# Optimization experiments

Hardware: AMD Instinct MI355X
Metric: run time of the kernel (lower is better)

Reference implementation:

```python
import jax, jax.numpy as jnp
import numpy as np

BOUND = 1.0
N_RAYS = 2048
TOT = 128        # num_steps (samples per pixel)
IND_S = 16       # indicator_steps
MAX_DEPTHS = 2
HID = 64
EPS = 1e-8


def setup_inputs() -> dict:
    key = jax.random.key(0)
    ks = jax.random.split(key, 13)
    M = N_RAYS * TOT
    rays_o = 0.3 * jax.random.normal(ks[0], (N_RAYS, 3), jnp.float32)
    rd = jax.random.normal(ks[1], (N_RAYS, 3), jnp.float32)
    rays_d = rd / (jnp.linalg.norm(rd, axis=-1, keepdims=True) + EPS)
    env_map = 0.1 * jax.random.normal(ks[2], (3, 128, 256), jnp.float32)
    Wd1 = jax.random.normal(ks[3], (3, HID), jnp.float32) / np.sqrt(3.0)
    Wd2 = jax.random.normal(ks[4], (HID, 3), jnp.float32) / np.sqrt(HID)
    Wf1 = jax.random.normal(ks[5], (6, HID), jnp.float32) / np.sqrt(6.0)
    Ws = jax.random.normal(ks[6], (HID, 3), jnp.float32) / np.sqrt(HID)
    Wdir = jax.random.normal(ks[7], (HID, 3), jnp.float32) / np.sqrt(HID)
    Wrho = jax.random.normal(ks[8], (HID, 3), jnp.float32) / np.sqrt(HID)
    jitter = jax.random.uniform(ks[9], (MAX_DEPTHS, M, IND_S), jnp.float32)
    u_t = jax.random.uniform(ks[10], (MAX_DEPTHS, M), jnp.float32)
    u_scatter = jax.random.uniform(ks[11], (MAX_DEPTHS, M), jnp.float32)
    channel = jax.random.randint(ks[12], (MAX_DEPTHS, M), 0, 3)
    return dict(rays_o=rays_o, rays_d=rays_d, env_map=env_map, Wd1=Wd1, Wd2=Wd2,
                Wf1=Wf1, Ws=Ws, Wdir=Wdir, Wrho=Wrho,
                jitter=jitter, u_t=u_t, u_scatter=u_scatter, channel=channel)


def _density(pts, Wd1, Wd2):
    # stand-in NeRF density field: 3 spectral channels, positive
    return jax.nn.softplus(jnp.sin(pts @ Wd1) @ Wd2)


def _material(o, d, Wf1, Ws, Wdir, Wrho):
    f = jnp.tanh(jnp.concatenate([o, d], axis=-1) @ Wf1)
    sigma_t = jax.nn.softplus(f @ Ws)                     # [M,3]
    dn = f @ Wdir
    d_out = dn / (jnp.linalg.norm(dn, axis=-1, keepdims=True) + EPS)
    fused_rho = jax.nn.sigmoid(f @ Wrho)                  # [M,3]
    return sigma_t, d_out, fused_rho


def _sample_env(env_map, p):
    # equirectangular lookup == torch grid_sample(bilinear, align_corners=False, zero pad)
    x, y, z = p[:, 0], p[:, 1], p[:, 2]
    theta = jnp.nan_to_num(jnp.arctan2(x, -z)) / jnp.pi            # grid x in [-1,1]
    phi = 2.0 / jnp.pi * jnp.nan_to_num(jnp.arccos(y)) - 1.0       # grid y in [-1,1]
    C, H, W = env_map.shape
    ix = ((theta + 1.0) * W - 1.0) * 0.5
    iy = ((phi + 1.0) * H - 1.0) * 0.5
    x0 = jnp.floor(ix); y0 = jnp.floor(iy)
    wx = ix - x0; wy = iy - y0

    def tap(xc, yc, w):
        inb = (xc >= 0) & (xc < W) & (yc >= 0) & (yc < H)
        xi = jnp.clip(xc, 0, W - 1).astype(jnp.int32)
        yi = jnp.clip(yc, 0, H - 1).astype(jnp.int32)
        return (w * inb)[:, None] * env_map[:, yi, xi].T   # [M,3]

    v = (tap(x0, y0, (1 - wx) * (1 - wy)) + tap(x0 + 1, y0, wx * (1 - wy)) +
         tap(x0, y0 + 1, (1 - wx) * wy) + tap(x0 + 1, y0 + 1, wx * wy))
    return jnp.exp(v)


def _render(rays_o, rays_d, env_map, Wd1, Wd2, Wf1, Ws, Wdir, Wrho,
            jitter, u_t, u_scatter, channel):
    M = N_RAYS * TOT
    o = jnp.repeat(rays_o, TOT, axis=0)   # [M,3]
    d = jnp.repeat(rays_d, TOT, axis=0)
    alive = jnp.ones((M,), bool)          # masked version of boolean compaction
    thr = jnp.ones((M, 3), jnp.float32)
    rgbs = jnp.zeros((M, 3), jnp.float32)
    lin = jnp.linspace(0.0, 1.0, IND_S)

    for dep in range(MAX_DEPTHS):
        # ray-sphere intersection (radius=bound)
        a = jnp.sum(d * d, -1)
        b = 2.0 * jnp.sum(d * o, -1)
        c = jnp.sum(o * o, -1) - BOUND ** 2
        delta = b * b - 4.0 * a * c
        alive = alive & (delta > 0.0)
        sq = jnp.sqrt(jnp.maximum(delta, 0.0))
        nears = jnp.maximum((-b - sq) / (2.0 * a), 0.001)
        fars = jnp.maximum((-b + sq) / (2.0 * a), 0.001)
        span = fars - nears

        # stratified indicator samples -> per-channel majorant
        z = nears[:, None] + span[:, None] * lin[None, :]
        z = z + (jitter[dep] - 0.5) * (span[:, None] / IND_S)
        pts = o[:, None, :] + d[:, None, :] * z[:, :, None]          # [M,S,3]
        sigma = _density(pts.reshape(-1, 3), Wd1, Wd2).reshape(M, IND_S, 3)
        ch = channel[dep]
        maj_multi = jnp.maximum(sigma.max(axis=1), 0.001)            # [M,3]
        sig_ch = jnp.take_along_axis(sigma, ch[:, None, None], axis=2)[..., 0]
        maj = jnp.maximum(sig_ch.max(axis=1), 0.001)                 # [M]

        # free-flight sampling (last depth forces hit at far boundary)
        if dep < MAX_DEPTHS - 1:
            t = -jnp.log1p(-u_t[dep]) / maj + nears
        else:
            t = fars
        hit = alive & (t >= fars)

        # environment hit contribution
        denom = jnp.exp(-maj_multi * span[:, None]) / (maj_multi.max(-1, keepdims=True) + EPS) + EPS
        Le = _sample_env(env_map, o + d * fars[:, None])
        contrib = thr * (denom / jax.lax.stop_gradient(denom.mean(-1, keepdims=True))) * Le
        rgbs = rgbs + jnp.where(hit[:, None], contrib, 0.0)
        alive = alive & ~hit
        if dep == MAX_DEPTHS - 1:
            break

        # throughput update + null/real scattering (delta tracking)
        trans = jnp.exp(-maj_multi * (t - nears)[:, None]) / maj_multi.max(-1, keepdims=True)
        den2 = jax.lax.stop_gradient((maj_multi * trans).mean(-1, keepdims=True))
        thr = jnp.where(alive[:, None], thr * trans / den2, thr)
        o = jnp.where(alive[:, None], jax.lax.stop_gradient(o + d * t[:, None]), o)
        sigma_t, d_out, fused_rho = _material(o, d, Wf1, Ws, Wdir, Wrho)
        sp = jnp.minimum(jnp.take_along_axis(sigma_t, ch[:, None], axis=1)[:, 0] / maj, 1.0)
        sm = alive & (u_scatter[dep] < sp)
        d = jnp.where(sm[:, None], d_out, d)
        thr = jnp.where(sm[:, None], thr / (sp[:, None] + EPS) * fused_rho,
              jnp.where(alive[:, None], thr / (1.0 - sp[:, None] + EPS), thr))

    return rgbs.reshape(N_RAYS, TOT, 3).mean(axis=1)   # [N,3]


def reference(rays_o, rays_d, env_map, Wd1, Wd2, Wf1, Ws, Wdir, Wrho,
              jitter, u_t, u_scatter, channel):
    return _render(rays_o, rays_d, env_map, Wd1, Wd2, Wf1, Ws, Wdir, Wrho,
                   jitter, u_t, u_scatter, channel)
```

## Files before the change

### kernel.cpp

```cpp
#include <hip/hip_runtime.h>
#include <math.h>

#define NRAYS 2048
#define TOT   128
#define INDS  16
#define HID   64
#define EPSF  1e-8f
#define MTOT  (NRAYS*TOT)
#define NTAB  128

typedef float f32x2 __attribute__((ext_vector_type(2)));
typedef float f32x4 __attribute__((ext_vector_type(4)));

__device__ __forceinline__ float softplus_f(float x) {
    return fmaxf(x, 0.0f) + __logf(1.0f + __expf(-fabsf(x)));
}
__device__ __forceinline__ float sigmoid_f(float x) {
    return 1.0f / (1.0f + __expf(-x));
}
__device__ __forceinline__ float tanh_fast(float x) {
    float e2 = __expf(2.0f * x);
    return 1.0f - 2.0f / (e2 + 1.0f);
}
__device__ __forceinline__ f32x2 pkmax(f32x2 a, f32x2 b) {
    f32x2 r; r.x = fmaxf(a.x, b.x); r.y = fmaxf(a.y, b.y); return r;
}
__device__ __forceinline__ f32x2 pkfma(f32x2 a, f32x2 b, f32x2 c) {
    return __builtin_elementwise_fma(a, b, c);
}

#define CK(i) ((float)(i)*(1.0f/15.0f) - 0.03125f)

#define MAKE_Z(jA, jB, kbase, nears, span)                                    \
    float s16 = (span) * (1.0f/16.0f);                                        \
    f32x2 z01, z23, z45, z67;                                                 \
    z01.x = fmaf((jA).x, s16, fmaf(span, CK((kbase)+0), nears));              \
    z01.y = fmaf((jA).y, s16, fmaf(span, CK((kbase)+1), nears));              \
    z23.x = fmaf((jA).z, s16, fmaf(span, CK((kbase)+2), nears));              \
    z23.y = fmaf((jA).w, s16, fmaf(span, CK((kbase)+3), nears));              \
    z45.x = fmaf((jB).x, s16, fmaf(span, CK((kbase)+4), nears));              \
    z45.y = fmaf((jB).y, s16, fmaf(span, CK((kbase)+5), nears));              \
    z67.x = fmaf((jB).z, s16, fmaf(span, CK((kbase)+6), nears));              \
    z67.y = fmaf((jB).w, s16, fmaf(span, CK((kbase)+7), nears));

#define TAB_EVAL(zz, mx0, mx1, mx2)                                           \
    {                                                                         \
        float x = ((zz) - ztab0) * invh;                                      \
        x = fminf(fmaxf(x, 0.0f), (float)(NTAB-1) - 1e-3f);                   \
        int i = (int)x; float w = x - (float)i;                               \
        float ta0 = sT0[i], tb0 = sT0[i+1];                                   \
        float ta1 = sT1[i], tb1 = sT1[i+1];                                   \
        float ta2 = sT2[i], tb2 = sT2[i+1];                                   \
        mx0 = fmaxf(mx0, fmaf(w, tb0 - ta0, ta0));                            \
        mx1 = fmaxf(mx1, fmaf(w, tb1 - ta1, ta1));                            \
        mx2 = fmaxf(mx2, fmaf(w, tb2 - ta2, ta2));                            \
    }

__device__ __forceinline__ void env_logv(
    const float* __restrict__ env_map,
    float px, float py, float pz,
    float& v0, float& v1, float& v2)
{
    float theta = atan2f(px, -pz) * (1.0f/3.14159265358979323846f);
    float acv = (fabsf(py) <= 1.0f) ? acosf(py) : 0.0f;
    float phi = 0.63661977236758134308f * acv - 1.0f;
    float ixf = ((theta + 1.0f)*256.0f - 1.0f)*0.5f;
    float iyf = ((phi   + 1.0f)*128.0f - 1.0f)*0.5f;
    float x0f = floorf(ixf), y0f = floorf(iyf);
    float wx = ixf - x0f, wy = iyf - y0f;
    v0 = 0.f; v1 = 0.f; v2 = 0.f;
    auto tap = [&](float xc, float yc, float w) {
        if (xc >= 0.0f && xc < 256.0f && yc >= 0.0f && yc < 128.0f) {
            int xi = (int)xc, yi = (int)yc;
            const float* e = env_map + yi*256 + xi;
            v0 += w * e[0];
            v1 += w * e[128*256];
            v2 += w * e[2*128*256];
        }
    };
    tap(x0f,      y0f,      (1.0f-wx)*(1.0f-wy));
    tap(x0f+1.0f, y0f,      wx*(1.0f-wy));
    tap(x0f,      y0f+1.0f, (1.0f-wx)*wy);
    tap(x0f+1.0f, y0f+1.0f, wx*wy);
}

__global__ __launch_bounds__(256)
void render_kernel(const float* __restrict__ rays_o,
                   const float* __restrict__ rays_d,
                   const float* __restrict__ env_map,
                   const float* __restrict__ Wd1,
                   const float* __restrict__ Wd2,
                   const float* __restrict__ Wf1,
                   const float* __restrict__ Ws,
                   const float* __restrict__ Wdir,
                   const float* __restrict__ Wrho,
                   const float* __restrict__ jitter,
                   const float* __restrict__ u_t,
                   const float* __restrict__ u_scatter,
                   const int*   __restrict__ channel,
                   float* __restrict__ out)
{
    const int ray  = blockIdx.x;
    const int tid  = threadIdx.x;
    const int s    = tid >> 1;
    const int half = tid & 1;
    const int m    = ray * TOT + s;
    const int kbase = half * 8;

    __shared__ f32x4 sAB[HID];
    __shared__ f32x4 sW01[HID];
    __shared__ f32x2 sW2[HID];
    __shared__ f32x4 sPW[HID];
    __shared__ f32x4 sM0[HID];
    __shared__ f32x4 sM1[HID];
    __shared__ f32x4 sM2[HID];
    __shared__ float sT0[NTAB];
    __shared__ float sT1[NTAB];
    __shared__ float sT2[NTAB];
    __shared__ f32x4 sP0[TOT];
    __shared__ f32x4 sP1[TOT];
    __shared__ f32x2 sP2[TOT];
    __shared__ float sEnvE[3];
    __shared__ int   sCnt;
    __shared__ float sred[4][3];

    const float4* j0p = (const float4*)(jitter + (size_t)m*INDS + kbase);
    float4 j0A = j0p[0], j0B = j0p[1];
    int   ch = channel[m];
    float ut = u_t[m];
    float us = u_scatter[m];

    float ox = rays_o[ray*3+0], oy = rays_o[ray*3+1], oz = rays_o[ray*3+2];
    float dx = rays_d[ray*3+0], dy = rays_d[ray*3+1], dz = rays_d[ray*3+2];

    if (tid == 0) sCnt = 0;
    if (tid < HID) {
        const float INV2PI = 0.15915494309189535f;
        float w1x = Wd1[tid], w1y = Wd1[HID+tid], w1z = Wd1[2*HID+tid];
        float pw1x = w1x*INV2PI, pw1y = w1y*INV2PI, pw1z = w1z*INV2PI;
        float A = ox*pw1x + oy*pw1y + oz*pw1z;
        float B = dx*pw1x + dy*pw1y + dz*pw1z;
        float w20 = Wd2[3*tid], w21 = Wd2[3*tid+1], w22 = Wd2[3*tid+2];
        sAB[tid]  = (f32x4){A, A, B, B};
        sW01[tid] = (f32x4){w20, w20, w21, w21};
        sW2[tid]  = (f32x2){w22, w22};
        sPW[tid]  = (f32x4){pw1x, pw1y, pw1z, 0.0f};
        float f0 = Wf1[tid],       f1 = Wf1[HID+tid],   f2 = Wf1[2*HID+tid];
        float f3 = Wf1[3*HID+tid], f4 = Wf1[4*HID+tid], f5 = Wf1[5*HID+tid];
        float P = ox*f0 + oy*f1 + oz*f2 + dx*f3 + dy*f4 + dz*f5;
        float Q = dx*f0 + dy*f1 + dz*f2;
        sM0[tid] = (f32x4){P, Q, Ws[3*tid], Ws[3*tid+1]};
        sM1[tid] = (f32x4){Ws[3*tid+2], Wdir[3*tid], Wdir[3*tid+1], Wdir[3*tid+2]};
        sM2[tid] = (f32x4){Wrho[3*tid], Wrho[3*tid+1], Wrho[3*tid+2], 0.0f};
    }
    __syncthreads();

    float a0g = dx*dx + dy*dy + dz*dz;
    float b0g = 2.0f*(dx*ox + dy*oy + dz*oz);
    float c0g = (ox*ox + oy*oy + oz*oz) - 1.0f;
    float delta0 = b0g*b0g - 4.0f*a0g*c0g;
    bool alive = (delta0 > 0.0f);

    float nears = 0.f, fars = 0.f, span = 0.f, ztab0 = 0.f, invh = 0.f;
    if (alive) {
        float sq = sqrtf(delta0);
        nears = fmaxf((-b0g - sq) / (2.0f*a0g), 0.001f);
        fars  = fmaxf((-b0g + sq) / (2.0f*a0g), 0.001f);
        span  = fars - nears;
        ztab0 = fmaf(-span, 0.03125f, nears);
        float width = span * 1.0625f;
        float hstep = width * (1.0f/(NTAB-1));
        invh = (float)(NTAB-1) / width;
        int p = tid >> 1;
        float zp = fmaf((float)p, hstep, ztab0);
        float f0 = 0.f, f1 = 0.f, f2 = 0.f;
        const int jb = half * 32;
        #pragma unroll 4
        for (int j = jb; j < jb + 32; ++j) {
            f32x4 ab  = sAB[j];
            f32x4 w01 = sW01[j];
            f32x2 w2  = sW2[j];
            float hv = __builtin_amdgcn_sinf(fmaf(zp, ab.z, ab.x));
            f0 = fmaf(hv, w01.x, f0);
            f1 = fmaf(hv, w01.z, f1);
            f2 = fmaf(hv, w2.x, f2);
        }
        f0 += __shfl_xor(f0, 1, 64);
        f1 += __shfl_xor(f1, 1, 64);
        f2 += __shfl_xor(f2, 1, 64);
        if (half == 0) { sT0[p] = f0; sT1[p] = f1; sT2[p] = f2; }
        if (tid == 0) {
            float v0,v1,v2;
            env_logv(env_map, fmaf(dx,fars,ox), fmaf(dy,fars,oy), fmaf(dz,fars,oz),
                     v0,v1,v2);
            sEnvE[0] = __expf(v0); sEnvE[1] = __expf(v1); sEnvE[2] = __expf(v2);
        }
    }
    __syncthreads();

    float thr0 = 1.f, thr1 = 1.f, thr2 = 1.f;
    float rgb0 = 0.f, rgb1 = 0.f, rgb2 = 0.f;
    bool  tab_d1 = false;
    float tadv = 0.f;

    if (alive) {
        MAKE_Z(j0A, j0B, kbase, nears, span)
        float mx0 = -1e30f, mx1 = -1e30f, mx2 = -1e30f;
        TAB_EVAL(z01.x, mx0,mx1,mx2) TAB_EVAL(z01.y, mx0,mx1,mx2)
        TAB_EVAL(z23.x, mx0,mx1,mx2) TAB_EVAL(z23.y, mx0,mx1,mx2)
        TAB_EVAL(z45.x, mx0,mx1,mx2) TAB_EVAL(z45.y, mx0,mx1,mx2)
        TAB_EVAL(z67.x, mx0,mx1,mx2) TAB_EVAL(z67.y, mx0,mx1,mx2)
        mx0 = fmaxf(mx0, __shfl_xor(mx0, 1, 64));
        mx1 = fmaxf(mx1, __shfl_xor(mx1, 1, 64));
        mx2 = fmaxf(mx2, __shfl_xor(mx2, 1, 64));

        float maj0 = fmaxf(softplus_f(mx0), 0.001f);
        float maj1 = fmaxf(softplus_f(mx1), 0.001f);
        float maj2 = fmaxf(softplus_f(mx2), 0.001f);
        float mmax = fmaxf(fmaxf(maj0, maj1), maj2);

        float maj = (ch == 0) ? maj0 : ((ch == 1) ? maj1 : maj2);
        float t   = -__logf(1.0f - ut) / maj + nears;

        if (t >= fars) {
            float den0 = __expf(-maj0*span)/(mmax+EPSF) + EPSF;
            float den1 = __expf(-maj1*span)/(mmax+EPSF) + EPSF;
            float den2 = __expf(-maj2*span)/(mmax+EPSF) + EPSF;
            float idm = 3.0f / (den0+den1+den2);
            rgb0 = den0*idm*sEnvE[0];
            rgb1 = den1*idm*sEnvE[1];
            rgb2 = den2*idm*sEnvE[2];
        } else {
            float tn  = t - nears;
            float imm = 1.0f / mmax;
            float tr0 = __expf(-maj0*tn) * imm;
            float tr1 = __expf(-maj1*tn) * imm;
            float tr2 = __expf(-maj2*tn) * imm;
            float i2m = 3.0f / (maj0*tr0 + maj1*tr1 + maj2*tr2);
            thr0 = tr0 * i2m;
            thr1 = tr1 * i2m;
            thr2 = tr2 * i2m;
            ox = fmaf(dx, t, ox); oy = fmaf(dy, t, oy); oz = fmaf(dz, t, oz);

            float st0=0.f, st1=0.f, st2=0.f;
            float dn0=0.f, dn1=0.f, dn2v=0.f;
            float rh0=0.f, rh1=0.f, rh2=0.f;
            const int j0 = half * 32;
            #pragma unroll 2
            for (int j = j0; j < j0 + 32; ++j) {
                f32x4 q0 = sM0[j];
                f32x4 q1 = sM1[j];
                f32x4 q2 = sM2[j];
                float pre = fmaf(t, q0.y, q0.x);
                float f = tanh_fast(pre);
                st0  = fmaf(f, q0.z, st0);
                st1  = fmaf(f, q0.w, st1);
                st2  = fmaf(f, q1.x, st2);
                dn0  = fmaf(f, q1.y, dn0);
                dn1  = fmaf(f, q1.z, dn1);
                dn2v = fmaf(f, q1.w, dn2v);
                rh0  = fmaf(f, q2.x, rh0);
                rh1  = fmaf(f, q2.y, rh1);
                rh2  = fmaf(f, q2.z, rh2);
            }
            st0  += __shfl_xor(st0, 1, 64);
            st1  += __shfl_xor(st1, 1, 64);
            st2  += __shfl_xor(st2, 1, 64);
            dn0  += __shfl_xor(dn0, 1, 64);
            dn1  += __shfl_xor(dn1, 1, 64);
            dn2v += __shfl_xor(dn2v, 1, 64);
            rh0  += __shfl_xor(rh0, 1, 64);
            rh1  += __shfl_xor(rh1, 1, 64);
            rh2  += __shfl_xor(rh2, 1, 64);

            float stch = (ch == 0) ? st0 : ((ch == 1) ? st1 : st2);
            float sp = fminf(softplus_f(stch) / maj, 1.0f);
            if (us < sp) {
                float inr = 1.0f / (sqrtf(dn0*dn0 + dn1*dn1 + dn2v*dn2v) + EPSF);
                float ndx = dn0*inr, ndy = dn1*inr, ndz = dn2v*inr;
                float isp = 1.0f/(sp + EPSF);
                float t0 = thr0 * isp * sigmoid_f(rh0);
                float t1 = thr1 * isp * sigmoid_f(rh1);
                float t2 = thr2 * isp * sigmoid_f(rh2);
                if (half == 0) {
                    int sl = atomicAdd(&sCnt, 1);
                    sP0[sl] = (f32x4){ox, oy, oz, ndx};
                    sP1[sl] = (f32x4){ndy, ndz, t0, t1};
                    sP2[sl] = (f32x2){t2, (float)m};
                }
            } else {
                float iv = 1.0f/(1.0f - sp + EPSF);
                thr0 *= iv; thr1 *= iv; thr2 *= iv;
                tab_d1 = true;
                tadv = t;
            }
        }
    }
    __syncthreads();
    int npool = sCnt;

    if (tab_d1) {
        float a1 = dx*dx + dy*dy + dz*dz;
        float b1 = 2.0f*(dx*ox + dy*oy + dz*oz);
        float c1 = (ox*ox + oy*oy + oz*oz) - 1.0f;
        float delta1 = b1*b1 - 4.0f*a1*c1;
        if (delta1 > 0.0f) {
            const float4* j1p = (const float4*)(jitter + ((size_t)MTOT + m)*INDS + kbase);
            float4 j1A = j1p[0], j1B = j1p[1];
            float sq1    = sqrtf(delta1);
            float nears1 = fmaxf((-b1 - sq1) / (2.0f*a1), 0.001f);
            float fars1  = fmaxf((-b1 + sq1) / (2.0f*a1), 0.001f);
            float span1  = fars1 - nears1;
            MAKE_Z(j1A, j1B, kbase, nears1, span1)
            float mx0 = -1e30f, mx1 = -1e30f, mx2 = -1e30f;
            TAB_EVAL(tadv + z01.x, mx0,mx1,mx2) TAB_EVAL(tadv + z01.y, mx0,mx1,mx2)
            TAB_EVAL(tadv + z23.x, mx0,mx1,mx2) TAB_EVAL(tadv + z23.y, mx0,mx1,mx2)
            TAB_EVAL(tadv + z45.x, mx0,mx1,mx2) TAB_EVAL(tadv + z45.y, mx0,mx1,mx2)
            TAB_EVAL(tadv + z67.x, mx0,mx1,mx2) TAB_EVAL(tadv + z67.y, mx0,mx1,mx2)
            mx0 = fmaxf(mx0, __shfl_xor(mx0, 1, 64));
            mx1 = fmaxf(mx1, __shfl_xor(mx1, 1, 64));
            mx2 = fmaxf(mx2, __shfl_xor(mx2, 1, 64));

            float maj0 = fmaxf(softplus_f(mx0), 0.001f);
            float maj1 = fmaxf(softplus_f(mx1), 0.001f);
            float maj2 = fmaxf(softplus_f(mx2), 0.001f);
            float mmax = fmaxf(fmaxf(maj0, maj1), maj2);

            float den0 = __expf(-maj0*span1)/(mmax+EPSF) + EPSF;
            float den1 = __expf(-maj1*span1)/(mmax+EPSF) + EPSF;
            float den2 = __expf(-maj2*span1)/(mmax+EPSF) + EPSF;
            float idm = 3.0f / (den0+den1+den2);
            rgb0 += thr0 * den0*idm*sEnvE[0];
            rgb1 += thr1 * den1*idm*sEnvE[1];
            rgb2 += thr2 * den2*idm*sEnvE[2];
        }
    }

    {
        const int qlane = tid & 3;
        const int kq    = qlane * 4;
        const float kqf = (float)kq;
        for (int q = tid >> 2; q < npool; q += 64) {
            f32x4 p0 = sP0[q];
            f32x4 p1 = sP1[q];
            f32x2 p2 = sP2[q];
            float pox = p0.x, poy = p0.y, poz = p0.z;
            float pdx = p0.w, pdy = p1.x, pdz = p1.y;
            float pt0 = p1.z, pt1 = p1.w, pt2 = p2.x;
            int   mm  = (int)p2.y;

            float a1 = pdx*pdx + pdy*pdy + pdz*pdz;
            float b1 = 2.0f*(pdx*pox + pdy*poy + pdz*poz);
            float c1 = (pox*pox + poy*poy + poz*poz) - 1.0f;
            float delta1 = b1*b1 - 4.0f*a1*c1;
            if (delta1 > 0.0f) {
                const float4* jp = (const float4*)(jitter + ((size_t)MTOT + mm)*INDS + kq);
                float4 jq = jp[0];
                float sq1    = sqrtf(delta1);
                float nears1 = fmaxf((-b1 - sq1) / (2.0f*a1), 0.001f);
                float fars1  = fmaxf((-b1 + sq1) / (2.0f*a1), 0.001f);
                float span1  = fars1 - nears1;
                float s16q   = span1 * (1.0f/16.0f);
                f32x2 zA, zB;
                zA.x = fmaf(jq.x, s16q, fmaf(span1, (kqf+0.0f)*(1.0f/15.0f) - 0.03125f, nears1));
                zA.y = fmaf(jq.y, s16q, fmaf(span1, (kqf+1.0f)*(1.0f/15.0f) - 0.03125f, nears1));
                zB.x = fmaf(jq.z, s16q, fmaf(span1, (kqf+2.0f)*(1.0f/15.0f) - 0.03125f, nears1));
                zB.y = fmaf(jq.w, s16q, fmaf(span1, (kqf+3.0f)*(1.0f/15.0f) - 0.03125f, nears1));

                f32x2 a0A = {0.f,0.f}, a0B = {0.f,0.f};
                f32x2 a1A = {0.f,0.f}, a1B = {0.f,0.f};
                f32x2 a2A = {0.f,0.f}, a2B = {0.f,0.f};
                #pragma unroll 2
                for (int j = 0; j < HID; ++j) {
                    f32x4 pw  = sPW[j];
                    f32x4 w01 = sW01[j];
                    f32x2 w2  = sW2[j];
                    float A = fmaf(pox, pw.x, fmaf(poy, pw.y, poz*pw.z));
                    float B = fmaf(pdx, pw.x, fmaf(pdy, pw.y, pdz*pw.z));
                    f32x2 A2 = {A, A}, B2 = {B, B};
                    f32x2 gA = pkfma(zA, B2, A2);
                    f32x2 gB = pkfma(zB, B2, A2);
                    f32x2 hA, hB;
                    hA.x = __builtin_amdgcn_sinf(gA.x); hA.y = __builtin_amdgcn_sinf(gA.y);
                    hB.x = __builtin_amdgcn_sinf(gB.x); hB.y = __builtin_amdgcn_sinf(gB.y);
                    f32x2 W0 = {w01.x, w01.y}, W1 = {w01.z, w01.w};
                    a0A = pkfma(hA, W0, a0A); a0B = pkfma(hB, W0, a0B);
                    a1A = pkfma(hA, W1, a1A); a1B = pkfma(hB, W1, a1B);
                    a2A = pkfma(hA, w2, a2A); a2B = pkfma(hB, w2, a2B);
                }
                f32x2 pm0 = pkmax(a0A, a0B);
                f32x2 pm1 = pkmax(a1A, a1B);
                f32x2 pm2 = pkmax(a2A, a2B);
                float mx0 = fmaxf(pm0.x, pm0.y);
                float mx1 = fmaxf(pm1.x, pm1.y);
                float mx2 = fmaxf(pm2.x, pm2.y);
                mx0 = fmaxf(mx0, __shfl_xor(mx0, 1, 64));
                mx1 = fmaxf(mx1, __shfl_xor(mx1, 1, 64));
                mx2 = fmaxf(mx2, __shfl_xor(mx2, 1, 64));
                mx0 = fmaxf(mx0, __shfl_xor(mx0, 2, 64));
                mx1 = fmaxf(mx1, __shfl_xor(mx1, 2, 64));
                mx2 = fmaxf(mx2, __shfl_xor(mx2, 2, 64));

                float maj0 = fmaxf(softplus_f(mx0), 0.001f);
                float maj1 = fmaxf(softplus_f(mx1), 0.001f);
                float maj2 = fmaxf(softplus_f(mx2), 0.001f);
                float mmax = fmaxf(fmaxf(maj0, maj1), maj2);

                float den0 = __expf(-maj0*span1)/(mmax+EPSF) + EPSF;
                float den1 = __expf(-maj1*span1)/(mmax+EPSF) + EPSF;
                float den2 = __expf(-maj2*span1)/(mmax+EPSF) + EPSF;
                float idm = 3.0f / (den0+den1+den2);
                float v0,v1,v2;
                env_logv(env_map, fmaf(pdx,fars1,pox), fmaf(pdy,fars1,poy),
                         fmaf(pdz,fars1,poz), v0,v1,v2);
                if (qlane < 2) {
                    rgb0 += pt0 * den0*idm*__expf(v0);
                    rgb1 += pt1 * den1*idm*__expf(v1);
                    rgb2 += pt2 * den2*idm*__expf(v2);
                }
            }
        }
    }

    float r0 = rgb0, r1 = rgb1, r2 = rgb2;
    #pragma unroll
    for (int off = 32; off > 0; off >>= 1) {
        r0 += __shfl_down(r0, off, 64);
        r1 += __shfl_down(r1, off, 64);
        r2 += __shfl_down(r2, off, 64);
    }
    int wave = tid >> 6;
    if ((tid & 63) == 0) {
        sred[wave][0] = r0; sred[wave][1] = r1; sred[wave][2] = r2;
    }
    __syncthreads();
    if (tid == 0) {
        out[ray*3+0] = (sred[0][0]+sred[1][0]+sred[2][0]+sred[3][0]) * (1.0f/256.0f);
        out[ray*3+1] = (sred[0][1]+sred[1][1]+sred[2][1]+sred[3][1]) * (1.0f/256.0f);
        out[ray*3+2] = (sred[0][2]+sred[1][2]+sred[2][2]+sred[3][2]) * (1.0f/256.0f);
    }
}

extern "C" void kernel_launch(void* const* d_in, const int* in_sizes, int n_in,
                              void* d_out, int out_size, void* d_ws, size_t ws_size,
                              hipStream_t stream) {
    const float* rays_o    = (const float*)d_in[0];
    const float* rays_d    = (const float*)d_in[1];
    const float* env_map   = (const float*)d_in[2];
    const float* Wd1       = (const float*)d_in[3];
    const float* Wd2       = (const float*)d_in[4];
    const float* Wf1       = (const float*)d_in[5];
    const float* Ws        = (const float*)d_in[6];
    const float* Wdir      = (const float*)d_in[7];
    const float* Wrho      = (const float*)d_in[8];
    const float* jitter    = (const float*)d_in[9];
    const float* u_t       = (const float*)d_in[10];
    const float* u_scatter = (const float*)d_in[11];
    const int*   channel   = (const int*)d_in[12];
    float* out = (float*)d_out;

    render_kernel<<<dim3(NRAYS), dim3(256), 0, stream>>>(
        rays_o, rays_d, env_map, Wd1, Wd2, Wf1, Ws, Wdir, Wrho,
        jitter, u_t, u_scatter, channel, out);
}
```

Before: 165.3 us.

## Read MLP weights directly from global memory and drop shared staging

Removes the per-block shared-memory staging of weight matrices and the sync that followed it, so every loop now reads Wd1/Wd2/Wf1/Ws/Wdir/Wrho straight from global memory. These loads are wave-uniform, so the compiler may turn them into scalar loads. The density table grows to 256 entries, computed by one thread per entry over all 64 hidden units instead of two threads splitting each entry. The material MLP is likewise computed whole by each thread, with no pairwise shuffle reduction. This trades LDS traffic and shuffles for global/scalar loads and duplicated work across the two half-threads. It also recomputes the material pre-activation from scratch instead of using precomputed P and Q.

```diff
diff --git a/kernel.cpp b/kernel.cpp
--- a/kernel.cpp
+++ b/kernel.cpp
@@ -7,7 +7,7 @@
 #define HID   64
 #define EPSF  1e-8f
 #define MTOT  (NRAYS*TOT)
-#define NTAB  128
+#define NTAB  256
 
 typedef float f32x2 __attribute__((ext_vector_type(2)));
 typedef float f32x4 __attribute__((ext_vector_type(4)));
@@ -106,14 +106,8 @@
     const int half = tid & 1;
     const int m    = ray * TOT + s;
     const int kbase = half * 8;
-
-    __shared__ f32x4 sAB[HID];
-    __shared__ f32x4 sW01[HID];
-    __shared__ f32x2 sW2[HID];
-    __shared__ f32x4 sPW[HID];
-    __shared__ f32x4 sM0[HID];
-    __shared__ f32x4 sM1[HID];
-    __shared__ f32x4 sM2[HID];
+    const float INV2PI = 0.15915494309189535f;
+
     __shared__ float sT0[NTAB];
     __shared__ float sT1[NTAB];
     __shared__ float sT2[NTAB];
@@ -134,26 +128,6 @@
     float dx = rays_d[ray*3+0], dy = rays_d[ray*3+1], dz = rays_d[ray*3+2];
 
     if (tid == 0) sCnt = 0;
-    if (tid < HID) {
-        const float INV2PI = 0.15915494309189535f;
-        float w1x = Wd1[tid], w1y = Wd1[HID+tid], w1z = Wd1[2*HID+tid];
-        float pw1x = w1x*INV2PI, pw1y = w1y*INV2PI, pw1z = w1z*INV2PI;
-        float A = ox*pw1x + oy*pw1y + oz*pw1z;
-        float B = dx*pw1x + dy*pw1y + dz*pw1z;
-        float w20 = Wd2[3*tid], w21 = Wd2[3*tid+1], w22 = Wd2[3*tid+2];
-        sAB[tid]  = (f32x4){A, A, B, B};
-        sW01[tid] = (f32x4){w20, w20, w21, w21};
-        sW2[tid]  = (f32x2){w22, w22};
-        sPW[tid]  = (f32x4){pw1x, pw1y, pw1z, 0.0f};
-        float f0 = Wf1[tid],       f1 = Wf1[HID+tid],   f2 = Wf1[2*HID+tid];
-        float f3 = Wf1[3*HID+tid], f4 = Wf1[4*HID+tid], f5 = Wf1[5*HID+tid];
-        float P = ox*f0 + oy*f1 + oz*f2 + dx*f3 + dy*f4 + dz*f5;
-        float Q = dx*f0 + dy*f1 + dz*f2;
-        sM0[tid] = (f32x4){P, Q, Ws[3*tid], Ws[3*tid+1]};
-        sM1[tid] = (f32x4){Ws[3*tid+2], Wdir[3*tid], Wdir[3*tid+1], Wdir[3*tid+2]};
-        sM2[tid] = (f32x4){Wrho[3*tid], Wrho[3*tid+1], Wrho[3*tid+2], 0.0f};
-    }
-    __syncthreads();
 
     float a0g = dx*dx + dy*dy + dz*dz;
     float b0g = 2.0f*(dx*ox + dy*oy + dz*oz);
@@ -171,24 +145,21 @@
         float width = span * 1.0625f;
         float hstep = width * (1.0f/(NTAB-1));
         invh = (float)(NTAB-1) / width;
-        int p = tid >> 1;
-        float zp = fmaf((float)p, hstep, ztab0);
+        float zp = fmaf((float)tid, hstep, ztab0);
         float f0 = 0.f, f1 = 0.f, f2 = 0.f;
-        const int jb = half * 32;
-        #pragma unroll 4
-        for (int j = jb; j < jb + 32; ++j) {
-            f32x4 ab  = sAB[j];
-            f32x4 w01 = sW01[j];
-            f32x2 w2  = sW2[j];
-            float hv = __builtin_amdgcn_sinf(fmaf(zp, ab.z, ab.x));
-            f0 = fmaf(hv, w01.x, f0);
-            f1 = fmaf(hv, w01.z, f1);
-            f2 = fmaf(hv, w2.x, f2);
-        }
-        f0 += __shfl_xor(f0, 1, 64);
-        f1 += __shfl_xor(f1, 1, 64);
-        f2 += __shfl_xor(f2, 1, 64);
-        if (half == 0) { sT0[p] = f0; sT1[p] = f1; sT2[p] = f2; }
+        float sox = ox*INV2PI, soy = oy*INV2PI, soz = oz*INV2PI;
+        float sdx = dx*INV2PI, sdy = dy*INV2PI, sdz = dz*INV2PI;
+        #pragma unroll 2
+        for (int j = 0; j < HID; ++j) {
+            float w1x = Wd1[j], w1y = Wd1[HID+j], w1z = Wd1[2*HID+j];
+            float A = fmaf(sox, w1x, fmaf(soy, w1y, soz*w1z));
+            float B = fmaf(sdx, w1x, fmaf(sdy, w1y, sdz*w1z));
+            float hv = __builtin_amdgcn_sinf(fmaf(zp, B, A));
+            f0 = fmaf(hv, Wd2[3*j+0], f0);
+            f1 = fmaf(hv, Wd2[3*j+1], f1);
+            f2 = fmaf(hv, Wd2[3*j+2], f2);
+        }
+        sT0[tid] = f0; sT1[tid] = f1; sT2[tid] = f2;
         if (tid == 0) {
             float v0,v1,v2;
             env_logv(env_map, fmaf(dx,fars,ox), fmaf(dy,fars,oy), fmaf(dz,fars,oz),
@@ -245,33 +216,23 @@
             float st0=0.f, st1=0.f, st2=0.f;
             float dn0=0.f, dn1=0.f, dn2v=0.f;
             float rh0=0.f, rh1=0.f, rh2=0.f;
-            const int j0 = half * 32;
             #pragma unroll 2
-            for (int j = j0; j < j0 + 32; ++j) {
-                f32x4 q0 = sM0[j];
-                f32x4 q1 = sM1[j];
-                f32x4 q2 = sM2[j];
-                float pre = fmaf(t, q0.y, q0.x);
+            for (int j = 0; j < HID; ++j) {
+                float f0 = Wf1[j],       f1 = Wf1[HID+j],   f2 = Wf1[2*HID+j];
+                float f3 = Wf1[3*HID+j], f4 = Wf1[4*HID+j], f5 = Wf1[5*HID+j];
+                float pre = fmaf(ox,f0, fmaf(oy,f1, fmaf(oz,f2,
+                            fmaf(dx,f3, fmaf(dy,f4, dz*f5)))));
                 float f = tanh_fast(pre);
-                st0  = fmaf(f, q0.z, st0);
-                st1  = fmaf(f, q0.w, st1);
-                st2  = fmaf(f, q1.x, st2);
-                dn0  = fmaf(f, q1.y, dn0);
-                dn1  = fmaf(f, q1.z, dn1);
-                dn2v = fmaf(f, q1.w, dn2v);
-                rh0  = fmaf(f, q2.x, rh0);
-                rh1  = fmaf(f, q2.y, rh1);
-                rh2  = fmaf(f, q2.z, rh2);
+                st0  = fmaf(f, Ws[3*j+0],   st0);
+                st1  = fmaf(f, Ws[3*j+1],   st1);
+                st2  = fmaf(f, Ws[3*j+2],   st2);
+                dn0  = fmaf(f, Wdir[3*j+0], dn0);
+                dn1  = fmaf(f, Wdir[3*j+1], dn1);
+                dn2v = fmaf(f, Wdir[3*j+2], dn2v);
+                rh0  = fmaf(f, Wrho[3*j+0], rh0);
+                rh1  = fmaf(f, Wrho[3*j+1], rh1);
+                rh2  = fmaf(f, Wrho[3*j+2], rh2);
             }
-            st0  += __shfl_xor(st0, 1, 64);
-            st1  += __shfl_xor(st1, 1, 64);
-            st2  += __shfl_xor(st2, 1, 64);
-            dn0  += __shfl_xor(dn0, 1, 64);
-            dn1  += __shfl_xor(dn1, 1, 64);
-            dn2v += __shfl_xor(dn2v, 1, 64);
-            rh0  += __shfl_xor(rh0, 1, 64);
-            rh1  += __shfl_xor(rh1, 1, 64);
-            rh2  += __shfl_xor(rh2, 1, 64);
 
             float stch = (ch == 0) ? st0 : ((ch == 1) ? st1 : st2);
             float sp = fminf(softplus_f(stch) / maj, 1.0f);
@@ -367,26 +328,28 @@
                 zB.x = fmaf(jq.z, s16q, fmaf(span1, (kqf+2.0f)*(1.0f/15.0f) - 0.03125f, nears1));
                 zB.y = fmaf(jq.w, s16q, fmaf(span1, (kqf+3.0f)*(1.0f/15.0f) - 0.03125f, nears1));
 
+                float sox = pox*INV2PI, soy = poy*INV2PI, soz = poz*INV2PI;
+                float sdx = pdx*INV2PI, sdy = pdy*INV2PI, sdz = pdz*INV2PI;
+
                 f32x2 a0A = {0.f,0.f}, a0B = {0.f,0.f};
                 f32x2 a1A = {0.f,0.f}, a1B = {0.f,0.f};
                 f32x2 a2A = {0.f,0.f}, a2B = {0.f,0.f};
                 #pragma unroll 2
                 for (int j = 0; j < HID; ++j) {
-                    f32x4 pw  = sPW[j];
-                    f32x4 w01 = sW01[j];
-                    f32x2 w2  = sW2[j];
-                    float A = fmaf(pox, pw.x, fmaf(poy, pw.y, poz*pw.z));
-                    float B = fmaf(pdx, pw.x, fmaf(pdy, pw.y, pdz*pw.z));
+                    float w1x = Wd1[j], w1y = Wd1[HID+j], w1z = Wd1[2*HID+j];
+                    float A = fmaf(sox, w1x, fmaf(soy, w1y, soz*w1z));
+                    float B = fmaf(sdx, w1x, fmaf(sdy, w1y, sdz*w1z));
                     f32x2 A2 = {A, A}, B2 = {B, B};
                     f32x2 gA = pkfma(zA, B2, A2);
                     f32x2 gB = pkfma(zB, B2, A2);
                     f32x2 hA, hB;
                     hA.x = __builtin_amdgcn_sinf(gA.x); hA.y = __builtin_amdgcn_sinf(gA.y);
                     hB.x = __builtin_amdgcn_sinf(gB.x); hB.y = __builtin_amdgcn_sinf(gB.y);
-                    f32x2 W0 = {w01.x, w01.y}, W1 = {w01.z, w01.w};
+                    float w20 = Wd2[3*j], w21 = Wd2[3*j+1], w22 = Wd2[3*j+2];
+                    f32x2 W0 = {w20, w20}, W1 = {w21, w21}, W2 = {w22, w22};
                     a0A = pkfma(hA, W0, a0A); a0B = pkfma(hB, W0, a0B);
                     a1A = pkfma(hA, W1, a1A); a1B = pkfma(hB, W1, a1B);
-                    a2A = pkfma(hA, w2, a2A); a2B = pkfma(hB, w2, a2B);
+                    a2A = pkfma(hA, W2, a2A); a2B = pkfma(hB, W2, a2B);
                 }
                 f32x2 pm0 = pkmax(a0A, a0B);
                 f32x2 pm1 = pkmax(a1A, a1B);
```

Result: slower. 185.6 us (+12.3%).
